# Kernel optimization log

Measured on AMD Instinct MI355X. Metric: run time of the kernel, lower is better.

The kernel has to match this reference:

```python
import jax, jax.numpy as jnp
import numpy as np

B, N, E, H = 4, 4096, 1024, 16
D = E // H


def setup_inputs() -> dict:
    key = jax.random.key(0)
    ks = jax.random.split(key, 8)
    s = 1.0 / np.sqrt(E)
    x = jax.random.normal(ks[0], (B, N, E), dtype=jnp.float32)
    # binary multiplicative sparsity pattern over the head-head score matrix
    sparsity_pattern = jax.random.randint(ks[1], (H, H), 0, 2).astype(jnp.float32)
    Wq = jax.random.normal(ks[2], (E, E), dtype=jnp.float32) * s
    bq = jax.random.normal(ks[3], (E,), dtype=jnp.float32) * s
    Wk = jax.random.normal(ks[4], (E, E), dtype=jnp.float32) * s
    bk = jax.random.normal(ks[5], (E,), dtype=jnp.float32) * s
    Wv = jax.random.normal(ks[6], (E, E), dtype=jnp.float32) * s
    bv = jax.random.normal(ks[7], (E,), dtype=jnp.float32) * s
    return {"x": x, "sparsity_pattern": sparsity_pattern,
            "Wq": Wq, "bq": bq, "Wk": Wk, "bk": bk, "Wv": Wv, "bv": bv}


def reference(x, sparsity_pattern, Wq, bq, Wk, bk, Wv, bv):
    b, n, e = x.shape
    # torch Linear: y = x @ W.T + b
    q = (x @ Wq.T + bq).reshape(b, n, H, D)
    k = (x @ Wk.T + bk).reshape(b, n, H, D)
    v = (x @ Wv.T + bv).reshape(b, n, H, D)
    # torch.matmul over last two dims of [B,N,H,D]: scores are [B,N,H,H]
    scores = jnp.einsum('bnhd,bngd->bnhg', q, k) * sparsity_pattern
    attn = jax.nn.softmax(scores, axis=-1)
    out = jnp.einsum('bnhg,bngd->bnhd', attn, v).reshape(b, n, e)
    return out
```

## Files before the change

### kernel.cpp

```cpp
#include <hip/hip_runtime.h>
#include <hip/hip_bf16.h>

#define M_   16384
#define K_   1024
#define NQKV 3072

typedef _Float16 f16x4 __attribute__((ext_vector_type(4)));
typedef _Float16 f16x8 __attribute__((ext_vector_type(8)));
typedef float    f32x4 __attribute__((ext_vector_type(4)));

__global__ __launch_bounds__(256) void cvt_f32_f16(const float* __restrict__ in,
                                                   _Float16* __restrict__ o, int n4) {
  int i = blockIdx.x * blockDim.x + threadIdx.x;
  const int stride = gridDim.x * blockDim.x;
  for (; i < n4; i += stride) {
    float4 v = ((const float4*)in)[i];
    f16x4 h; h[0] = (_Float16)v.x; h[1] = (_Float16)v.y;
    h[2] = (_Float16)v.z; h[3] = (_Float16)v.w;
    *(f16x4*)&o[(size_t)i * 4] = h;
  }
}

__global__ __launch_bounds__(256) void cvt3_f32_f16(
    const float* __restrict__ a, const float* __restrict__ b,
    const float* __restrict__ c, _Float16* __restrict__ o, int n4each) {
  const float* src = (blockIdx.y == 0) ? a : (blockIdx.y == 1) ? b : c;
  _Float16* dst = o + (size_t)blockIdx.y * n4each * 4;
  int i = blockIdx.x * blockDim.x + threadIdx.x;
  const int stride = gridDim.x * blockDim.x;
  for (; i < n4each; i += stride) {
    float4 v = ((const float4*)src)[i];
    f16x4 h; h[0] = (_Float16)v.x; h[1] = (_Float16)v.y;
    h[2] = (_Float16)v.z; h[3] = (_Float16)v.w;
    *(f16x4*)&dst[(size_t)i * 4] = h;
  }
}

__global__ __launch_bounds__(512, 2) void gemm_qkv(
    const _Float16* __restrict__ xh, const _Float16* __restrict__ wh,
    const float* __restrict__ bq, const float* __restrict__ bk,
    const float* __restrict__ bv, _Float16* __restrict__ qkv)
{
  __shared__ __align__(16) _Float16 As[2][256 * 64];
  __shared__ __align__(16) _Float16 Bs[2][256 * 64];

  const int tid  = threadIdx.x;
  const int ln   = tid & 63;
  const int w    = tid >> 6;
  const int wm2  = w >> 2;
  const int wn4  = w & 3;
  const int lcol = ln & 15, quad = ln >> 4;

  const int bid = blockIdx.x;
  const int swz = (bid & 7) * 96 + (bid >> 3);
  const int m0 = (swz / 12) * 256;
  const int n0 = (swz % 12) * 256;

  f32x4 acc[8][4];
#pragma unroll
  for (int i = 0; i < 8; ++i)
#pragma unroll
    for (int j = 0; j < 4; ++j) acc[i][j] = f32x4{0.f, 0.f, 0.f, 0.f};

  f16x8 a0[4][2], a1[4][2], b0[2][2], b1[2][2];

#define STAGE_A(BUF, KT, X)                                                    \
  { _Pragma("unroll")                                                          \
    for (int j = 0; j < 2; ++j) {                                              \
      const int c   = j * 512 + tid;                                           \
      const int rr  = c >> 3;                                                  \
      const int r   = (X) * 64 + (rr & 63) + ((rr >> 6) << 7);                 \
      const int cb  = (c & 7) ^ (r & 7);                                       \
      const int rr0 = j * 64 + w * 8;                                          \
      const int r0  = (X) * 64 + (rr0 & 63) + ((rr0 >> 6) << 7);               \
      __builtin_amdgcn_global_load_lds(                                        \
          (const __attribute__((address_space(1))) void*)(                     \
              xh + (size_t)(m0 + r) * K_ + (KT) * 64 + cb * 8),                \
          (__attribute__((address_space(3))) void*)(&As[BUF][r0 * 64]),        \
          16, 0, 0);                                                           \
    } }

#define STAGE_B(BUF, KT, Y)                                                    \
  { _Pragma("unroll")                                                          \
    for (int j = 0; j < 2; ++j) {                                              \
      const int c   = j * 512 + tid;                                           \
      const int rr  = c >> 3;                                                  \
      const int r   = ((rr >> 5) << 6) + (Y) * 32 + (rr & 31);                 \
      const int cb  = (c & 7) ^ (r & 7);                                       \
      const int rr0 = j * 64 + w * 8;                                          \
      const int r0  = ((rr0 >> 5) << 6) + (Y) * 32 + (rr0 & 31);               \
      __builtin_amdgcn_global_load_lds(                                        \
          (const __attribute__((address_space(1))) void*)(                     \
              wh + (size_t)(n0 + r) * K_ + (KT) * 64 + cb * 8),                \
          (__attribute__((address_space(3))) void*)(&Bs[BUF][r0 * 64]),        \
          16, 0, 0);                                                           \
    } }

#define RDA(DST, BUF, MH)                                                      \
  _Pragma("unroll")                                                            \
  for (int mi = 0; mi < 4; ++mi) {                                             \
    const int ar = wm2 * 128 + (MH) * 64 + mi * 16 + lcol;                     \
    const int sw = ar & 7;                                                     \
    DST[mi][0] = *(const f16x8*)&As[BUF][ar * 64 + ((quad    ) ^ sw) * 8];     \
    DST[mi][1] = *(const f16x8*)&As[BUF][ar * 64 + ((quad + 4) ^ sw) * 8];     \
  }

#define RDB(DST, BUF, NH)                                                      \
  _Pragma("unroll")                                                            \
  for (int ni = 0; ni < 2; ++ni) {                                             \
    const int br = wn4 * 64 + (NH) * 32 + ni * 16 + lcol;                      \
    const int sw = br & 7;                                                     \
    DST[ni][0] = *(const f16x8*)&Bs[BUF][br * 64 + ((quad    ) ^ sw) * 8];     \
    DST[ni][1] = *(const f16x8*)&Bs[BUF][br * 64 + ((quad + 4) ^ sw) * 8];     \
  }

#define MFMA16(AARR, BARR, MH, NH)                                             \
  __builtin_amdgcn_s_setprio(1);                                               \
  _Pragma("unroll")                                                            \
  for (int kb = 0; kb < 2; ++kb)                                               \
    _Pragma("unroll")                                                          \
    for (int mi = 0; mi < 4; ++mi)                                             \
      _Pragma("unroll")                                                        \
      for (int ni = 0; ni < 2; ++ni)                                           \
        acc[(MH) * 4 + mi][(NH) * 2 + ni] =                                    \
            __builtin_amdgcn_mfma_f32_16x16x32_f16(                            \
                AARR[mi][kb], BARR[ni][kb], acc[(MH) * 4 + mi][(NH) * 2 + ni], \
                0, 0, 0);                                                      \
  __builtin_amdgcn_s_setprio(0);

#define SB()    __builtin_amdgcn_sched_barrier(0)
#define BAR()   { __builtin_amdgcn_s_barrier(); SB(); }
#define LGKM(N) { asm volatile("s_waitcnt lgkmcnt(" #N ")" ::: "memory"); SB(); }
#define VM0()   { asm volatile("s_waitcnt vmcnt(0)" ::: "memory"); SB(); }

#define KTILE(CUR, T, NOTLAST)                                                 \
  { \
    RDB(b0, CUR, 0); SB();                                                     \
    RDA(a0, CUR, 0); SB();                                                     \
    RDA(a1, CUR, 1); SB();                                                     \
    RDB(b1, CUR, 1); SB();                                                     \
    if (NOTLAST) {                                                             \
      STAGE_A(1 - (CUR), (T) + 1, 0); STAGE_B(1 - (CUR), (T) + 1, 0);          \
      STAGE_A(1 - (CUR), (T) + 1, 1); STAGE_B(1 - (CUR), (T) + 1, 1);          \
      SB();                                                                    \
    }                                                                          \
    LGKM(12); MFMA16(a0, b0, 0, 0);                                            \
    LGKM(4);  MFMA16(a1, b0, 1, 0);                                            \
    LGKM(0);  MFMA16(a1, b1, 1, 1);                                            \
              MFMA16(a0, b1, 0, 1);                                            \
    if (NOTLAST) { VM0(); }                                                    \
    BAR();                                                                     \
  }

  STAGE_A(0, 0, 0); STAGE_B(0, 0, 0); STAGE_A(0, 0, 1); STAGE_B(0, 0, 1);
  VM0(); BAR();

#pragma unroll 1
  for (int it = 0; it < 7; ++it) {
    KTILE(0, it * 2,     1);
    KTILE(1, it * 2 + 1, 1);
  }
  KTILE(0, 14, 1);
  KTILE(1, 15, 0);

  float bi4[4];
#pragma unroll
  for (int nh = 0; nh < 4; ++nh) {
    const int col = n0 + wn4 * 64 + nh * 16 + lcol;
    const int seg = col >> 10, cs = col & 1023;
    bi4[nh] = ((seg == 0) ? bq : (seg == 1) ? bk : bv)[cs];
  }
#pragma unroll
  for (int mi = 0; mi < 8; ++mi) {
    const int r0 = m0 + wm2 * 128 + mi * 16 + quad * 4;
#pragma unroll
    for (int r = 0; r < 4; ++r) {
      _Float16* rowp = qkv + (size_t)(r0 + r) * 3072 + n0 + wn4 * 64 + lcol;
#pragma unroll
      for (int nh = 0; nh < 4; ++nh)
        rowp[nh * 16] = (_Float16)(acc[mi][nh][r] + bi4[nh]);
    }
  }
#undef STAGE_A
#undef STAGE_B
#undef RDA
#undef RDB
#undef MFMA16
#undef SB
#undef BAR
#undef LGKM
#undef VM0
#undef KTILE
}

__global__ __launch_bounds__(256) void attn_kernel(
    const _Float16* __restrict__ qkv,
    const float* __restrict__ pat,
    float* __restrict__ out)
{
  __shared__ __align__(16) _Float16 Ps[4][16 * 24];
  __shared__ __align__(16) _Float16 Vt[4][64 * 24];

  const int tid  = threadIdx.x;
  const int ln   = tid & 63;
  const int wv   = tid >> 6;
  const int lcol = ln & 15, quad = ln >> 4;
  const int t    = blockIdx.x * 4 + wv;

  const _Float16* qg = qkv + (size_t)t * 3072;
  const _Float16* kg = qg + 1024;
  const _Float16* vg = qg + 2048;

  f16x8 vc[2];
  vc[0] = *(const f16x8*)(vg + ((ln >> 3)    ) * 64 + (ln & 7) * 8);
  vc[1] = *(const f16x8*)(vg + ((ln >> 3) + 8) * 64 + (ln & 7) * 8);
  f16x8 aq0 = *(const f16x8*)(qg + lcol * 64 + quad * 8);
  f16x8 aq1 = *(const f16x8*)(qg + lcol * 64 + 32 + quad * 8);
  f16x8 bk0 = *(const f16x8*)(kg + lcol * 64 + quad * 8);
  f16x8 bk1 = *(const f16x8*)(kg + lcol * 64 + 32 + quad * 8);
  float p4[4];
#pragma unroll
  for (int r = 0; r < 4; r++) p4[r] = pat[(quad * 4 + r) * 16 + lcol];

#pragma unroll
  for (int i = 0; i < 2; i++) {
    const int g = (ln >> 3) + i * 8, c = (ln & 7) * 8;
#pragma unroll
    for (int j = 0; j < 8; j++) Vt[wv][(c + j) * 24 + g] = vc[i][j];
  }

  f32x4 s = {0.f, 0.f, 0.f, 0.f};
  s = __builtin_amdgcn_mfma_f32_16x16x32_f16(aq0, bk0, s, 0, 0, 0);
  s = __builtin_amdgcn_mfma_f32_16x16x32_f16(aq1, bk1, s, 0, 0, 0);

#pragma unroll
  for (int r = 0; r < 4; r++) {
    const float sv = s[r] * p4[r];
    float m = sv;
#pragma unroll
    for (int msk = 1; msk < 16; msk <<= 1) m = fmaxf(m, __shfl_xor(m, msk, 64));
    const float e = __expf(sv - m);
    float su = e;
#pragma unroll
    for (int msk = 1; msk < 16; msk <<= 1) su += __shfl_xor(su, msk, 64);
    Ps[wv][(quad * 4 + r) * 24 + lcol] = (_Float16)(e / su);
  }

  f16x4 ap = *(const f16x4*)&Ps[wv][lcol * 24 + quad * 4];

  f32x4 o[4];
#pragma unroll
  for (int dt = 0; dt < 4; dt++) {
    f16x4 bvf = *(const f16x4*)&Vt[wv][(dt * 16 + lcol) * 24 + quad * 4];
    f32x4 z = {0.f, 0.f, 0.f, 0.f};
    o[dt] = __builtin_amdgcn_mfma_f32_16x16x16f16(ap, bvf, z, 0, 0, 0);
  }

  float* op = out + (size_t)t * 1024;
#pragma unroll
  for (int r = 0; r < 4; r++) {
    float* rp = op + (quad * 4 + r) * 64 + lcol;
#pragma unroll
    for (int dt = 0; dt < 4; dt++)
      rp[dt * 16] = o[dt][r];
  }
}

extern "C" void kernel_launch(void* const* d_in, const int* in_sizes, int n_in,
                              void* d_out, int out_size, void* d_ws, size_t ws_size,
                              hipStream_t stream) {
  const float* x   = (const float*)d_in[0];
  const float* pat = (const float*)d_in[1];
  const float* Wq  = (const float*)d_in[2];
  const float* bq  = (const float*)d_in[3];
  const float* Wk  = (const float*)d_in[4];
  const float* bk  = (const float*)d_in[5];
  const float* Wv  = (const float*)d_in[6];
  const float* bv  = (const float*)d_in[7];

  _Float16* qkvh = (_Float16*)d_ws;
  _Float16* xh   = qkvh + (size_t)50331648;
  _Float16* wh   = qkvh + (size_t)67108864;

  cvt_f32_f16<<<4096, 256, 0, stream>>>(x, xh, 4194304);
  cvt3_f32_f16<<<dim3(256, 3), 256, 0, stream>>>(Wq, Wk, Wv, wh, 262144);

  gemm_qkv<<<768, 512, 0, stream>>>(xh, wh, bq, bk, bv, qkvh);
  attn_kernel<<<M_ / 4, 256, 0, stream>>>(qkvh, pat, (float*)d_out);
}
```

Before: 297.9 us.

## Halve GEMM K-tile to 32 and merge fp32-to-fp16 conversion kernels

The QKV GEMM now stages K-tiles of 32 instead of 64, which halves LDS use per buffer (64KB to 32KB total). It uses a simpler 4-way XOR swizzle and a single B fragment set reused across both A halves, and doubles the number of k-iterations. Separately, the x and weight conversion kernels are merged into one launch to save one kernel launch. The smaller tile may allow better occupancy but adds more barriers and waits per unit of work.

```diff
diff --git a/kernel.cpp b/kernel.cpp
--- a/kernel.cpp
+++ b/kernel.cpp
@@ -9,30 +9,24 @@
 typedef _Float16 f16x8 __attribute__((ext_vector_type(8)));
 typedef float    f32x4 __attribute__((ext_vector_type(4)));
 
-__global__ __launch_bounds__(256) void cvt_f32_f16(const float* __restrict__ in,
-                                                   _Float16* __restrict__ o, int n4) {
+__global__ __launch_bounds__(256) void cvt_all(
+    const float* __restrict__ x,  const float* __restrict__ Wq,
+    const float* __restrict__ Wk, const float* __restrict__ Wv,
+    _Float16* __restrict__ xh, _Float16* __restrict__ wh) {
   int i = blockIdx.x * blockDim.x + threadIdx.x;
   const int stride = gridDim.x * blockDim.x;
-  for (; i < n4; i += stride) {
-    float4 v = ((const float4*)in)[i];
+  for (; i < 4980736; i += stride) {
+    const float* src; _Float16* dst; int idx;
+    if (i < 4194304) { src = x; dst = xh; idx = i; }
+    else {
+      const int j = i - 4194304, sel = j >> 18; idx = j & 262143;
+      src = (sel == 0) ? Wq : (sel == 1) ? Wk : Wv;
+      dst = wh + (size_t)sel * 1048576;
+    }
+    float4 v = ((const float4*)src)[idx];
     f16x4 h; h[0] = (_Float16)v.x; h[1] = (_Float16)v.y;
     h[2] = (_Float16)v.z; h[3] = (_Float16)v.w;
-    *(f16x4*)&o[(size_t)i * 4] = h;
-  }
-}
-
-__global__ __launch_bounds__(256) void cvt3_f32_f16(
-    const float* __restrict__ a, const float* __restrict__ b,
-    const float* __restrict__ c, _Float16* __restrict__ o, int n4each) {
-  const float* src = (blockIdx.y == 0) ? a : (blockIdx.y == 1) ? b : c;
-  _Float16* dst = o + (size_t)blockIdx.y * n4each * 4;
-  int i = blockIdx.x * blockDim.x + threadIdx.x;
-  const int stride = gridDim.x * blockDim.x;
-  for (; i < n4each; i += stride) {
-    float4 v = ((const float4*)src)[i];
-    f16x4 h; h[0] = (_Float16)v.x; h[1] = (_Float16)v.y;
-    h[2] = (_Float16)v.z; h[3] = (_Float16)v.w;
-    *(f16x4*)&dst[(size_t)i * 4] = h;
+    *(f16x4*)&dst[(size_t)idx * 4] = h;
   }
 }
 
@@ -41,8 +35,8 @@
     const float* __restrict__ bq, const float* __restrict__ bk,
     const float* __restrict__ bv, _Float16* __restrict__ qkv)
 {
-  __shared__ __align__(16) _Float16 As[2][256 * 64];
-  __shared__ __align__(16) _Float16 Bs[2][256 * 64];
+  __shared__ __align__(16) _Float16 As[2][256 * 32];
+  __shared__ __align__(16) _Float16 Bs[2][256 * 32];
 
   const int tid  = threadIdx.x;
   const int ln   = tid & 63;
@@ -62,70 +56,43 @@
 #pragma unroll
     for (int j = 0; j < 4; ++j) acc[i][j] = f32x4{0.f, 0.f, 0.f, 0.f};
 
-  f16x8 a0[4][2], a1[4][2], b0[2][2], b1[2][2];
-
-#define STAGE_A(BUF, KT, X)                                                    \
+  f16x8 alo[4], ahi[4], b[4];
+
+#define STAGE32(BUF, T, GPTR, ROW0, LDSARR)                                    \
   { _Pragma("unroll")                                                          \
     for (int j = 0; j < 2; ++j) {                                              \
-      const int c   = j * 512 + tid;                                           \
-      const int rr  = c >> 3;                                                  \
-      const int r   = (X) * 64 + (rr & 63) + ((rr >> 6) << 7);                 \
-      const int cb  = (c & 7) ^ (r & 7);                                       \
-      const int rr0 = j * 64 + w * 8;                                          \
-      const int r0  = (X) * 64 + (rr0 & 63) + ((rr0 >> 6) << 7);               \
+      const int c  = j * 512 + tid;                                            \
+      const int r  = c >> 2;                                                   \
+      const int cb = (c & 3) ^ (r & 3);                                        \
       __builtin_amdgcn_global_load_lds(                                        \
           (const __attribute__((address_space(1))) void*)(                     \
-              xh + (size_t)(m0 + r) * K_ + (KT) * 64 + cb * 8),                \
-          (__attribute__((address_space(3))) void*)(&As[BUF][r0 * 64]),        \
+              GPTR + (size_t)((ROW0) + r) * K_ + (T) * 32 + cb * 8),           \
+          (__attribute__((address_space(3))) void*)(                           \
+              &LDSARR[BUF][(j * 512 + w * 64) * 8]),                           \
           16, 0, 0);                                                           \
     } }
 
-#define STAGE_B(BUF, KT, Y)                                                    \
-  { _Pragma("unroll")                                                          \
-    for (int j = 0; j < 2; ++j) {                                              \
-      const int c   = j * 512 + tid;                                           \
-      const int rr  = c >> 3;                                                  \
-      const int r   = ((rr >> 5) << 6) + (Y) * 32 + (rr & 31);                 \
-      const int cb  = (c & 7) ^ (r & 7);                                       \
-      const int rr0 = j * 64 + w * 8;                                          \
-      const int r0  = ((rr0 >> 5) << 6) + (Y) * 32 + (rr0 & 31);               \
-      __builtin_amdgcn_global_load_lds(                                        \
-          (const __attribute__((address_space(1))) void*)(                     \
-              wh + (size_t)(n0 + r) * K_ + (KT) * 64 + cb * 8),                \
-          (__attribute__((address_space(3))) void*)(&Bs[BUF][r0 * 64]),        \
-          16, 0, 0);                                                           \
-    } }
-
-#define RDA(DST, BUF, MH)                                                      \
+#define RDB(BUF)                                                               \
+  _Pragma("unroll")                                                            \
+  for (int ni = 0; ni < 4; ++ni) {                                             \
+    const int br = wn4 * 64 + ni * 16 + lcol;                                  \
+    b[ni] = *(const f16x8*)&Bs[BUF][br * 32 + ((quad ^ (br & 3))) * 8];        \
+  }
+#define RDA(DST, BUF, H)                                                       \
   _Pragma("unroll")                                                            \
   for (int mi = 0; mi < 4; ++mi) {                                             \
-    const int ar = wm2 * 128 + (MH) * 64 + mi * 16 + lcol;                     \
-    const int sw = ar & 7;                                                     \
-    DST[mi][0] = *(const f16x8*)&As[BUF][ar * 64 + ((quad    ) ^ sw) * 8];     \
-    DST[mi][1] = *(const f16x8*)&As[BUF][ar * 64 + ((quad + 4) ^ sw) * 8];     \
-  }
-
-#define RDB(DST, BUF, NH)                                                      \
-  _Pragma("unroll")                                                            \
-  for (int ni = 0; ni < 2; ++ni) {                                             \
-    const int br = wn4 * 64 + (NH) * 32 + ni * 16 + lcol;                      \
-    const int sw = br & 7;                                                     \
-    DST[ni][0] = *(const f16x8*)&Bs[BUF][br * 64 + ((quad    ) ^ sw) * 8];     \
-    DST[ni][1] = *(const f16x8*)&Bs[BUF][br * 64 + ((quad + 4) ^ sw) * 8];     \
-  }
-
-#define MFMA16(AARR, BARR, MH, NH)                                             \
+    const int ar = wm2 * 128 + (H) * 64 + mi * 16 + lcol;                      \
+    DST[mi] = *(const f16x8*)&As[BUF][ar * 32 + ((quad ^ (ar & 3))) * 8];      \
+  }
+
+#define MFMA16(AARR, H)                                                        \
   __builtin_amdgcn_s_setprio(1);                                               \
   _Pragma("unroll")                                                            \
-  for (int kb = 0; kb < 2; ++kb)                                               \
+  for (int mi = 0; mi < 4; ++mi)                                               \
     _Pragma("unroll")                                                          \
-    for (int mi = 0; mi < 4; ++mi)                                             \
-      _Pragma("unroll")                                                        \
-      for (int ni = 0; ni < 2; ++ni)                                           \
-        acc[(MH) * 4 + mi][(NH) * 2 + ni] =                                    \
-            __builtin_amdgcn_mfma_f32_16x16x32_f16(                            \
-                AARR[mi][kb], BARR[ni][kb], acc[(MH) * 4 + mi][(NH) * 2 + ni], \
-                0, 0, 0);                                                      \
+    for (int ni = 0; ni < 4; ++ni)                                             \
+      acc[(H) * 4 + mi][ni] = __builtin_amdgcn_mfma_f32_16x16x32_f16(          \
+          AARR[mi], b[ni], acc[(H) * 4 + mi][ni], 0, 0, 0);                    \
   __builtin_amdgcn_s_setprio(0);
 
 #define SB()    __builtin_amdgcn_sched_barrier(0)
@@ -134,57 +101,48 @@
 #define VM0()   { asm volatile("s_waitcnt vmcnt(0)" ::: "memory"); SB(); }
 
 #define KTILE(CUR, T, NOTLAST)                                                 \
-  { \
-    RDB(b0, CUR, 0); SB();                                                     \
-    RDA(a0, CUR, 0); SB();                                                     \
-    RDA(a1, CUR, 1); SB();                                                     \
-    RDB(b1, CUR, 1); SB();                                                     \
+  { RDB(CUR); RDA(alo, CUR, 0); RDA(ahi, CUR, 1); SB();          \
     if (NOTLAST) {                                                             \
-      STAGE_A(1 - (CUR), (T) + 1, 0); STAGE_B(1 - (CUR), (T) + 1, 0);          \
-      STAGE_A(1 - (CUR), (T) + 1, 1); STAGE_B(1 - (CUR), (T) + 1, 1);          \
-      SB();                                                                    \
+      STAGE32(1 - (CUR), (T) + 1, xh, m0, As);                                 \
+      STAGE32(1 - (CUR), (T) + 1, wh, n0, Bs); SB();                           \
     }                                                                          \
-    LGKM(12); MFMA16(a0, b0, 0, 0);                                            \
-    LGKM(4);  MFMA16(a1, b0, 1, 0);                                            \
-    LGKM(0);  MFMA16(a1, b1, 1, 1);                                            \
-              MFMA16(a0, b1, 0, 1);                                            \
+    LGKM(4); MFMA16(alo, 0);           \
+    LGKM(0); MFMA16(ahi, 1);                                                   \
     if (NOTLAST) { VM0(); }                                                    \
-    BAR();                                                                     \
-  }
-
-  STAGE_A(0, 0, 0); STAGE_B(0, 0, 0); STAGE_A(0, 0, 1); STAGE_B(0, 0, 1);
+    BAR(); }
+
+  STAGE32(0, 0, xh, m0, As); STAGE32(0, 0, wh, n0, Bs);
   VM0(); BAR();
 
 #pragma unroll 1
-  for (int it = 0; it < 7; ++it) {
+  for (int it = 0; it < 15; ++it) {
     KTILE(0, it * 2,     1);
     KTILE(1, it * 2 + 1, 1);
   }
-  KTILE(0, 14, 1);
-  KTILE(1, 15, 0);
+  KTILE(0, 30, 1);
+  KTILE(1, 31, 0);
 
   float bi4[4];
 #pragma unroll
-  for (int nh = 0; nh < 4; ++nh) {
-    const int col = n0 + wn4 * 64 + nh * 16 + lcol;
+  for (int nt = 0; nt < 4; ++nt) {
+    const int col = n0 + wn4 * 64 + nt * 16 + lcol;
     const int seg = col >> 10, cs = col & 1023;
-    bi4[nh] = ((seg == 0) ? bq : (seg == 1) ? bk : bv)[cs];
-  }
-#pragma unroll
-  for (int mi = 0; mi < 8; ++mi) {
-    const int r0 = m0 + wm2 * 128 + mi * 16 + quad * 4;
+    bi4[nt] = ((seg == 0) ? bq : (seg == 1) ? bk : bv)[cs];
+  }
+#pragma unroll
+  for (int mt = 0; mt < 8; ++mt) {
+    const int r0 = m0 + wm2 * 128 + mt * 16 + quad * 4;
 #pragma unroll
     for (int r = 0; r < 4; ++r) {
       _Float16* rowp = qkv + (size_t)(r0 + r) * 3072 + n0 + wn4 * 64 + lcol;
 #pragma unroll
-      for (int nh = 0; nh < 4; ++nh)
-        rowp[nh * 16] = (_Float16)(acc[mi][nh][r] + bi4[nh]);
+      for (int nt = 0; nt < 4; ++nt)
+        rowp[nt * 16] = (_Float16)(acc[mt][nt][r] + bi4[nt]);
     }
   }
-#undef STAGE_A
-#undef STAGE_B
+#undef STAGE32
+#undef RDB
 #undef RDA
-#undef RDB
 #undef MFMA16
 #undef SB
 #undef BAR
@@ -282,8 +240,7 @@
   _Float16* xh   = qkvh + (size_t)50331648;
   _Float16* wh   = qkvh + (size_t)67108864;
 
-  cvt_f32_f16<<<4096, 256, 0, stream>>>(x, xh, 4194304);
-  cvt3_f32_f16<<<dim3(256, 3), 256, 0, stream>>>(Wq, Wk, Wv, wh, 262144);
+  cvt_all<<<4096, 256, 0, stream>>>(x, Wq, Wk, Wv, xh, wh);
 
   gemm_qkv<<<768, 512, 0, stream>>>(xh, wh, bq, bk, bv, qkvh);
   attn_kernel<<<M_ / 4, 256, 0, stream>>>(qkvh, pat, (float*)d_out);
```

Measured after the change: 268.4 us. 9.9% less time.
